# Kernel tuning notes

Hardware: AMD Instinct MI355X
Metric: run time of the kernel (lower is better)

## Reference

```python
import jax, jax.numpy as jnp
import numpy as np


def setup_inputs() -> dict:
    key = jax.random.key(0)
    k1, k2, k3 = jax.random.split(key, 3)
    B, N, M, KSUB, DSUB = 32, 1_000_000, 64, 256, 4
    querys = jax.random.normal(k1, (B, M * DSUB), dtype=jnp.float32)
    codewords = jax.random.normal(k2, (M, KSUB, DSUB), dtype=jnp.float32)
    codes = jax.random.randint(k3, (N, M), 0, KSUB, dtype=jnp.int32)
    return {"querys": querys, "codewords": codewords, "codes": codes, "k": 64}


def reference(querys, codewords, codes, k):
    """PQ asymmetric-distance (ADC) search, metric='l2'.

    querys:    (B, D) with D = M*dsub
    codewords: (M, ksub, dsub)
    codes:     (N, M) byte codes (int32 here)
    Returns (topk_distances (B,k), topk_indices (B,k)) -- smallest L2 first,
    matching faiss IndexPQ semantics.
    """
    B, D = querys.shape
    M, KSUB, DSUB = codewords.shape
    N = codes.shape[0]
    # Per-subspace squared-L2 distance table: (B, M, ksub)
    q = querys.reshape(B, M, 1, DSUB)
    table = jnp.sum((q - codewords[None]) ** 2, axis=-1)

    # ADC scan: dist[b, n] = sum_m table[b, m, codes[n, m]].
    # Loop over the M subspaces (structural dim) via lax.scan to avoid
    # materializing a (B, N, M) intermediate.
    table_m_first = jnp.transpose(table, (1, 0, 2))  # (M, B, ksub)
    codes_m_first = codes.T                          # (M, N)

    def step(acc, inp):
        t_m, c_m = inp  # (B, ksub), (N,)
        return acc + t_m[:, c_m], None  # gather -> (B, N)

    init = jnp.zeros((B, N), dtype=querys.dtype)
    dists, _ = jax.lax.scan(step, init, (table_m_first, codes_m_first))

    neg_top, idx = jax.lax.top_k(-dists, k)  # k nearest (smallest L2)
    return -neg_top, idx
```

## Files before the change

### kernel.cpp

```cpp
#include <hip/hip_runtime.h>
#include <cstdint>


#define BQ 32
#define MSUB 64
#define KSUB 256
#define DSUB 4
#define KOUT 64
#define NSAMP 16384
#define TAU_RANK 24
#define CAP 16384
#define NSORT 4096

__global__ __launch_bounds__(256) void build_table(const float* __restrict__ q,
                                                   const float* __restrict__ cw,
                                                   float* __restrict__ table) {
    int tid = blockIdx.x * 256 + threadIdx.x;
    int b = tid & 31;
    int c = (tid >> 5) & 255;
    int m = tid >> 13;
    const float* qp = q + b * (MSUB * DSUB) + m * DSUB;
    const float* cp = cw + (m * KSUB + c) * DSUB;
    float s = 0.f;
#pragma unroll
    for (int d = 0; d < DSUB; ++d) { float t = qp[d] - cp[d]; s += t * t; }
    table[tid] = s;
}

__global__ __launch_bounds__(256) void sample_dists(const float* __restrict__ table,
                                                    const int* __restrict__ codes,
                                                    float* __restrict__ samp,
                                                    int stride, int offset) {
    int j = blockIdx.x * 256 + threadIdx.x;
    int n = j * stride + offset;
    const int* crow = codes + (long)n * MSUB;
    float acc[BQ];
#pragma unroll
    for (int b = 0; b < BQ; ++b) acc[b] = 0.f;
    for (int m = 0; m < MSUB; ++m) {
        int c = crow[m];
        const float* t = table + (m * KSUB + c) * BQ;
#pragma unroll
        for (int b = 0; b < BQ; ++b) acc[b] += t[b];
    }
#pragma unroll
    for (int b = 0; b < BQ; ++b) samp[b * NSAMP + j] = acc[b];
}

__global__ __launch_bounds__(256) void find_tau(const float* __restrict__ samp,
                                                float* __restrict__ tau) {
    __shared__ uint32_t sbits[NSAMP];
    __shared__ int scount;
    int b = blockIdx.x;
    for (int i = threadIdx.x; i < NSAMP; i += 256)
        sbits[i] = __float_as_uint(samp[b * NSAMP + i]);
    __syncthreads();
    uint32_t lo = 0u, hi = 0x7F800000u;
    for (int it = 0; it < 31; ++it) {
        uint32_t mid = (lo + hi) >> 1;
        if (threadIdx.x == 0) scount = 0;
        __syncthreads();
        int c = 0;
        for (int i = threadIdx.x; i < NSAMP; i += 256) c += (sbits[i] <= mid) ? 1 : 0;
        atomicAdd(&scount, c);
        __syncthreads();
        int cnt = scount;
        __syncthreads();
        if (cnt >= TAU_RANK) hi = mid; else lo = mid;
    }
    if (threadIdx.x == 0) tau[b] = __uint_as_float(hi);
}

__global__ __launch_bounds__(256) void scan_collect(const float* __restrict__ table,
                                                    const int* __restrict__ codes,
                                                    const float* __restrict__ tau,
                                                    int* __restrict__ cnt,
                                                    int* __restrict__ cidx,
                                                    float* __restrict__ cdist,
                                                    int N) {
    int tid = blockIdx.x * 256 + threadIdx.x;
    int n = tid >> 3;
    if (n >= N) return;
    int q4 = tid & 7;
    const int* crow = codes + (long)n * MSUB;
    const float4* t4 = (const float4*)table;
    float4 acc = {0.f, 0.f, 0.f, 0.f};
#pragma unroll 8
    for (int m = 0; m < MSUB; ++m) {
        int c = crow[m];
        float4 v = t4[(m * KSUB + c) * 8 + q4];
        acc.x += v.x; acc.y += v.y; acc.z += v.z; acc.w += v.w;
    }
    float d[4] = {acc.x, acc.y, acc.z, acc.w};
    int b0 = q4 * 4;
#pragma unroll
    for (int j = 0; j < 4; ++j) {
        int b = b0 + j;
        if (d[j] <= tau[b]) {
            int pos = atomicAdd(&cnt[b], 1);
            if (pos < CAP) { cidx[b * CAP + pos] = n; cdist[b * CAP + pos] = d[j]; }
        }
    }
}

__global__ __launch_bounds__(256) void final_topk(const int* __restrict__ cnt,
                                                  const int* __restrict__ cidx,
                                                  const float* __restrict__ cdist,
                                                  float* __restrict__ out) {
    __shared__ unsigned long long keys[NSORT];
    int b = blockIdx.x;
    int m = cnt[b];
    if (m > NSORT) m = NSORT;
    for (int i = threadIdx.x; i < NSORT; i += 256) {
        unsigned long long k;
        if (i < m)
            k = ((unsigned long long)__float_as_uint(cdist[b * CAP + i]) << 32) |
                (unsigned int)cidx[b * CAP + i];
        else
            k = ~0ULL;
        keys[i] = k;
    }
    __syncthreads();
    for (int kk = 2; kk <= NSORT; kk <<= 1) {
        for (int j = kk >> 1; j > 0; j >>= 1) {
            for (int i = threadIdx.x; i < NSORT; i += 256) {
                int ixj = i ^ j;
                if (ixj > i) {
                    unsigned long long a = keys[i], c = keys[ixj];
                    bool up = ((i & kk) == 0);
                    if ((a > c) == up) { keys[i] = c; keys[ixj] = a; }
                }
            }
            __syncthreads();
        }
    }
    for (int r = threadIdx.x; r < KOUT; r += 256) {
        unsigned long long k = keys[r];
        out[b * KOUT + r] = __uint_as_float((unsigned int)(k >> 32));
        out[BQ * KOUT + b * KOUT + r] = (float)(unsigned int)(k & 0xFFFFFFFFu);
    }
}

extern "C" void kernel_launch(void* const* d_in, const int* in_sizes, int n_in,
                              void* d_out, int out_size, void* d_ws, size_t ws_size,
                              hipStream_t stream) {
    const float* querys    = (const float*)d_in[0];
    const float* codewords = (const float*)d_in[1];
    const int*   codes     = (const int*)d_in[2];
    float* out = (float*)d_out;
    int N = in_sizes[2] / MSUB;

    char* ws = (char*)d_ws;
    float* table = (float*)(ws);
    float* samp  = (float*)(ws + (2u << 20));
    float* tau   = (float*)(ws + (4u << 20));
    int*   cnt   = (int*)  (ws + (4u << 20) + 4096);
    int*   cidx  = (int*)  (ws + (4u << 20) + 8192);
    float* cdist = (float*)(ws + (6u << 20) + 8192);

    hipMemsetAsync(cnt, 0, BQ * sizeof(int), stream);

    build_table<<<(MSUB * KSUB * BQ) / 256, 256, 0, stream>>>(querys, codewords, table);

    int stride = N / NSAMP;
    int offset = 17;
    sample_dists<<<NSAMP / 256, 256, 0, stream>>>(table, codes, samp, stride, offset);

    find_tau<<<BQ, 256, 0, stream>>>(samp, tau);

    long total = (long)N * 8;
    int blocks = (int)((total + 255) / 256);
    scan_collect<<<blocks, 256, 0, stream>>>(table, codes, tau, cnt, cidx, cdist, N);

    final_topk<<<BQ, 256, 0, stream>>>(cnt, cidx, cdist, out);
}
```

Baseline: 653.8 us.

## Use 8-bit quantized LDS lookup tables with SWAR coarse scan plus exact refine

The codes are repacked into a transposed byte layout each call. The distance table is quantized to 8-bit per subspace and query, and the full scan becomes an LDS-resident SWAR filter: two 16-bit lanes are accumulated per 32-bit word, and each candidate is compared against a quantized, slack-padded threshold. Surviving candidates are rescored exactly from the float table before the final bitonic sort. This aims to replace the costly per-row global float4 gathers with cheap shared-memory byte lookups, at the cost of extra passes over the codes. It also risks exceeding the candidate cap, because quantization slack lets extra candidates through the coarse filter.

```diff
diff --git a/kernel.cpp b/kernel.cpp
--- a/kernel.cpp
+++ b/kernel.cpp
@@ -7,10 +7,26 @@
 #define KSUB 256
 #define DSUB 4
 #define KOUT 64
-#define NSAMP 16384
-#define TAU_RANK 24
-#define CAP 16384
-#define NSORT 4096
+#define NSAMP 8192
+#define TAU_RANK 12
+#define CAP 8192
+#define NSORT 8192
+#define CHUNK_N 2048
+
+__device__ __forceinline__ unsigned pack4(int4 a) {
+    return (unsigned)(a.x & 255) | ((unsigned)(a.y & 255) << 8) |
+           ((unsigned)(a.z & 255) << 16) | ((unsigned)(a.w & 255) << 24);
+}
+__global__ __launch_bounds__(256) void pack_codes_t(const int4* __restrict__ c4,
+                                                    uint4* __restrict__ PT, int N) {
+    int t = blockIdx.x * 256 + threadIdx.x;
+    if (t >= N * 4) return;
+    int n = t >> 2, w = t & 3;
+    const int4* src = c4 + ((long)n * 16 + w * 4);
+    uint4 r;
+    r.x = pack4(src[0]); r.y = pack4(src[1]); r.z = pack4(src[2]); r.w = pack4(src[3]);
+    PT[(long)(n >> 6) * 256 + w * 64 + (n & 63)] = r;
+}
 
 __global__ __launch_bounds__(256) void build_table(const float* __restrict__ q,
                                                    const float* __restrict__ cw,
@@ -27,6 +43,66 @@
     table[tid] = s;
 }
 
+__global__ __launch_bounds__(256) void minmax_kernel(const float* __restrict__ table,
+                                                     float* __restrict__ off,
+                                                     unsigned* __restrict__ maxr) {
+    int m = blockIdx.x >> 5, b = blockIdx.x & 31;
+    int c = threadIdx.x;
+    float v = table[(m * 256 + c) * 32 + b];
+    __shared__ float smin[256], smax[256];
+    smin[c] = v; smax[c] = v;
+    __syncthreads();
+    for (int s = 128; s > 0; s >>= 1) {
+        if (c < s) {
+            smin[c] = fminf(smin[c], smin[c + s]);
+            smax[c] = fmaxf(smax[c], smax[c + s]);
+        }
+        __syncthreads();
+    }
+    if (c == 0) {
+        off[m * 32 + b] = smin[0];
+        atomicMax(&maxr[b], __float_as_uint(smax[0] - smin[0]));
+    }
+}
+
+__global__ __launch_bounds__(64) void scale_kernel(const float* __restrict__ off,
+                                                   const unsigned* __restrict__ maxr,
+                                                   float* __restrict__ sVal,
+                                                   float* __restrict__ OFFv) {
+    int b = threadIdx.x;
+    if (b >= BQ) return;
+    float r = __uint_as_float(maxr[b]);
+    if (r < 1e-20f) r = 1e-20f;
+    sVal[b] = 254.5f / r;
+    float o = 0.f;
+    for (int m = 0; m < MSUB; ++m) o += off[m * 32 + b];
+    OFFv[b] = o;
+}
+
+__global__ __launch_bounds__(256) void quantize_table(const float* __restrict__ table,
+                                                      const float* __restrict__ off,
+                                                      const float* __restrict__ sVal,
+                                                      unsigned* __restrict__ qg) {
+    int m = blockIdx.x, c = threadIdx.x;
+    const float* t = table + (m * 256 + c) * 32;
+    unsigned q[32];
+#pragma unroll
+    for (int b = 0; b < 32; ++b) {
+        float x = floorf((t[b] - off[m * 32 + b]) * sVal[b]);
+        int qi = (int)x;
+        if (qi < 0) qi = 0;
+        if (qi > 255) qi = 255;
+        q[b] = (unsigned)qi;
+    }
+#pragma unroll
+    for (int o = 0; o < 4; ++o) {
+        unsigned A = q[o*8+0] | (q[o*8+1] << 8) | (q[o*8+2] << 16) | (q[o*8+3] << 24);
+        unsigned B = q[o*8+4] | (q[o*8+5] << 8) | (q[o*8+6] << 16) | (q[o*8+7] << 24);
+        qg[(2 * o + 0) * 16384 + m * 256 + c] = A;
+        qg[(2 * o + 1) * 16384 + m * 256 + c] = B;
+    }
+}
+
 __global__ __launch_bounds__(256) void sample_dists(const float* __restrict__ table,
                                                     const int* __restrict__ codes,
                                                     float* __restrict__ samp,
@@ -49,15 +125,15 @@
 
 __global__ __launch_bounds__(256) void find_tau(const float* __restrict__ samp,
                                                 float* __restrict__ tau) {
-    __shared__ uint32_t sbits[NSAMP];
+    __shared__ unsigned sbits[NSAMP];
     __shared__ int scount;
     int b = blockIdx.x;
     for (int i = threadIdx.x; i < NSAMP; i += 256)
         sbits[i] = __float_as_uint(samp[b * NSAMP + i]);
     __syncthreads();
-    uint32_t lo = 0u, hi = 0x7F800000u;
+    unsigned lo = 0u, hi = 0x7F800000u;
     for (int it = 0; it < 31; ++it) {
-        uint32_t mid = (lo + hi) >> 1;
+        unsigned mid = (lo + hi) >> 1;
         if (threadIdx.x == 0) scount = 0;
         __syncthreads();
         int c = 0;
@@ -71,36 +147,118 @@
     if (threadIdx.x == 0) tau[b] = __uint_as_float(hi);
 }
 
-__global__ __launch_bounds__(256) void scan_collect(const float* __restrict__ table,
-                                                    const int* __restrict__ codes,
-                                                    const float* __restrict__ tau,
-                                                    int* __restrict__ cnt,
-                                                    int* __restrict__ cidx,
-                                                    float* __restrict__ cdist,
-                                                    int N) {
-    int tid = blockIdx.x * 256 + threadIdx.x;
-    int n = tid >> 3;
-    if (n >= N) return;
-    int q4 = tid & 7;
-    const int* crow = codes + (long)n * MSUB;
-    const float4* t4 = (const float4*)table;
-    float4 acc = {0.f, 0.f, 0.f, 0.f};
-#pragma unroll 8
-    for (int m = 0; m < MSUB; ++m) {
-        int c = crow[m];
-        float4 v = t4[(m * KSUB + c) * 8 + q4];
-        acc.x += v.x; acc.y += v.y; acc.z += v.z; acc.w += v.w;
-    }
-    float d[4] = {acc.x, acc.y, acc.z, acc.w};
-    int b0 = q4 * 4;
-#pragma unroll
-    for (int j = 0; j < 4; ++j) {
-        int b = b0 + j;
-        if (d[j] <= tau[b]) {
-            int pos = atomicAdd(&cnt[b], 1);
-            if (pos < CAP) { cidx[b * CAP + pos] = n; cdist[b * CAP + pos] = d[j]; }
-        }
-    }
+__global__ __launch_bounds__(64) void qtau_kernel(const float* __restrict__ tau,
+                                                  const float* __restrict__ sVal,
+                                                  const float* __restrict__ OFFv,
+                                                  unsigned* __restrict__ Qt) {
+    int b = threadIdx.x;
+    if (b >= BQ) return;
+    float x = (tau[b] - OFFv[b]) * sVal[b];
+    int q = (int)floorf(x) + 8;
+    if (q < 0) q = 0;
+    if (q > 65535) q = 65535;
+    Qt[b] = (unsigned)q;
+}
+
+__global__ __launch_bounds__(512) void coarse_scan(const unsigned* __restrict__ qg,
+                                                   const uint4* __restrict__ PT,
+                                                   const unsigned* __restrict__ Qt,
+                                                   int* __restrict__ cnt,
+                                                   int* __restrict__ cidx,
+                                                   int N) {
+    __shared__ unsigned qlds[32768];
+    int o = blockIdx.y;
+    {
+        const uint4* src = (const uint4*)(qg + 2 * o * 16384);
+        uint4* dst = (uint4*)qlds;
+        for (int i = threadIdx.x; i < 8192; i += 512) dst[i] = src[i];
+    }
+    unsigned Tp0, Tp1, Tp2, Tp3, Tp4, Tp5, Tp6, Tp7;
+    {
+        const unsigned* qb = Qt + o * 8;
+        Tp0 = min(qb[0] + 1u, 32767u); Tp1 = min(qb[1] + 1u, 32767u);
+        Tp2 = min(qb[2] + 1u, 32767u); Tp3 = min(qb[3] + 1u, 32767u);
+        Tp4 = min(qb[4] + 1u, 32767u); Tp5 = min(qb[5] + 1u, 32767u);
+        Tp6 = min(qb[6] + 1u, 32767u); Tp7 = min(qb[7] + 1u, 32767u);
+    }
+    unsigned TloA = Tp0 | (Tp2 << 16), ThiA = Tp1 | (Tp3 << 16);
+    unsigned TloB = Tp4 | (Tp6 << 16), ThiB = Tp5 | (Tp7 << 16);
+    __syncthreads();
+
+    int n0 = blockIdx.x * CHUNK_N;
+    for (int i = threadIdx.x; i < CHUNK_N; i += 512) {
+        int n = n0 + i;
+        if (n >= N) break;
+        const uint4* p = PT + ((long)(n >> 6) * 256 + (n & 63));
+        uint4 w0 = p[0], w1 = p[64], w2 = p[128], w3 = p[192];
+        unsigned cw[16] = {w0.x, w0.y, w0.z, w0.w, w1.x, w1.y, w1.z, w1.w,
+                           w2.x, w2.y, w2.z, w2.w, w3.x, w3.y, w3.z, w3.w};
+        unsigned a0 = 0, a1 = 0, a2 = 0, a3 = 0;
+#pragma unroll
+        for (int w = 0; w < 16; ++w) {
+            unsigned word = cw[w];
+#pragma unroll
+            for (int k = 0; k < 4; ++k) {
+                int m = w * 4 + k;
+                unsigned c = (word >> (8 * k)) & 255u;
+                unsigned vA = qlds[m * 256 + c];
+                unsigned vB = qlds[16384 + m * 256 + c];
+                a0 += vA & 0x00FF00FFu;
+                a1 += (vA >> 8) & 0x00FF00FFu;
+                a2 += vB & 0x00FF00FFu;
+                a3 += (vB >> 8) & 0x00FF00FFu;
+            }
+        }
+        unsigned d0 = (a0 | 0x80008000u) - TloA;
+        unsigned d1 = (a1 | 0x80008000u) - ThiA;
+        unsigned d2 = (a2 | 0x80008000u) - TloB;
+        unsigned d3 = (a3 | 0x80008000u) - ThiB;
+        unsigned any = (~d0 | ~d1 | ~d2 | ~d3) & 0x80008000u;
+        if (any) {
+#pragma unroll
+            for (int j = 0; j < 8; ++j) {
+                unsigned src = (j < 4) ? ((j & 1) ? a1 : a0) : ((j & 1) ? a3 : a2);
+                unsigned v = (j & 2) ? (src >> 16) : (src & 0xFFFFu);
+                unsigned T = (j == 0) ? Tp0 : (j == 1) ? Tp1 : (j == 2) ? Tp2 :
+                             (j == 3) ? Tp3 : (j == 4) ? Tp4 : (j == 5) ? Tp5 :
+                             (j == 6) ? Tp6 : Tp7;
+                if (v < T) {
+                    int b = o * 8 + j;
+                    int pos = atomicAdd(&cnt[b], 1);
+                    if (pos < CAP) cidx[b * CAP + pos] = n;
+                }
+            }
+        }
+    }
+}
+
+__global__ __launch_bounds__(256) void refine(const float* __restrict__ table,
+                                              const uint4* __restrict__ PT,
+                                              const int* __restrict__ cnt,
+                                              const int* __restrict__ cidx,
+                                              float* __restrict__ cdist) {
+    int b = blockIdx.y;
+    int pos = blockIdx.x * 256 + threadIdx.x;
+    int mc = cnt[b]; if (mc > CAP) mc = CAP;
+    if (pos >= mc) return;
+    int n = cidx[b * CAP + pos];
+    const uint4* p = PT + ((long)(n >> 6) * 256 + (n & 63));
+    uint4 w0 = p[0], w1 = p[64], w2 = p[128], w3 = p[192];
+    unsigned cw[16] = {w0.x, w0.y, w0.z, w0.w, w1.x, w1.y, w1.z, w1.w,
+                       w2.x, w2.y, w2.z, w2.w, w3.x, w3.y, w3.z, w3.w};
+    float s = 0.f;
+    const float* tb = table + b;
+#pragma unroll
+    for (int w = 0; w < 16; ++w) {
+        unsigned word = cw[w];
+#pragma unroll
+        for (int k = 0; k < 4; ++k) {
+            unsigned c = (word >> (8 * k)) & 255u;
+            int m = w * 4 + k;
+            s += tb[(m * 256 + c) * 32];
+        }
+    }
+    cdist[b * CAP + pos] = s;
 }
 
 __global__ __launch_bounds__(256) void final_topk(const int* __restrict__ cnt,
@@ -115,7 +273,7 @@
         unsigned long long k;
         if (i < m)
             k = ((unsigned long long)__float_as_uint(cdist[b * CAP + i]) << 32) |
-                (unsigned int)cidx[b * CAP + i];
+                (unsigned)cidx[b * CAP + i];
         else
             k = ~0ULL;
         keys[i] = k;
@@ -136,8 +294,8 @@
     }
     for (int r = threadIdx.x; r < KOUT; r += 256) {
         unsigned long long k = keys[r];
-        out[b * KOUT + r] = __uint_as_float((unsigned int)(k >> 32));
-        out[BQ * KOUT + b * KOUT + r] = (float)(unsigned int)(k & 0xFFFFFFFFu);
+        out[b * KOUT + r] = __uint_as_float((unsigned)(k >> 32));
+        out[BQ * KOUT + b * KOUT + r] = (float)(unsigned)(k & 0xFFFFFFFFu);
     }
 }
 
@@ -151,26 +309,42 @@
     int N = in_sizes[2] / MSUB;
 
     char* ws = (char*)d_ws;
-    float* table = (float*)(ws);
-    float* samp  = (float*)(ws + (2u << 20));
-    float* tau   = (float*)(ws + (4u << 20));
-    int*   cnt   = (int*)  (ws + (4u << 20) + 4096);
-    int*   cidx  = (int*)  (ws + (4u << 20) + 8192);
-    float* cdist = (float*)(ws + (6u << 20) + 8192);
-
-    hipMemsetAsync(cnt, 0, BQ * sizeof(int), stream);
+    float*    table = (float*)(ws);
+    float*    samp  = (float*)(ws + (2u << 20));
+    char*     small = ws + (3u << 20);
+    float*    tau   = (float*)(small + 0);
+    float*    sVal  = (float*)(small + 128);
+    float*    OFFv  = (float*)(small + 256);
+    unsigned* Qt    = (unsigned*)(small + 384);
+    int*      cnt   = (int*)(small + 512);
+    unsigned* maxr  = (unsigned*)(small + 640);
+    float*    off   = (float*)(small + 1024);
+    unsigned* qg    = (unsigned*)(small + 16384);
+    int*      cidx  = (int*)(ws + (4u << 20));
+    float*    cdist = (float*)(ws + (5u << 20));
+    uint4*    PT    = (uint4*)(ws + (6u << 20));
+
+    hipMemsetAsync(small + 512, 0, 256, stream);
+
+    pack_codes_t<<<(N * 4) / 256 + 1, 256, 0, stream>>>((const int4*)codes, PT, N);
 
     build_table<<<(MSUB * KSUB * BQ) / 256, 256, 0, stream>>>(querys, codewords, table);
+
+    minmax_kernel<<<MSUB * BQ, 256, 0, stream>>>(table, off, maxr);
+    scale_kernel<<<1, 64, 0, stream>>>(off, maxr, sVal, OFFv);
+    quantize_table<<<MSUB, 256, 0, stream>>>(table, off, sVal, qg);
 
     int stride = N / NSAMP;
     int offset = 17;
     sample_dists<<<NSAMP / 256, 256, 0, stream>>>(table, codes, samp, stride, offset);
-
     find_tau<<<BQ, 256, 0, stream>>>(samp, tau);
-
-    long total = (long)N * 8;
-    int blocks = (int)((total + 255) / 256);
-    scan_collect<<<blocks, 256, 0, stream>>>(table, codes, tau, cnt, cidx, cdist, N);
+    qtau_kernel<<<1, 64, 0, stream>>>(tau, sVal, OFFv, Qt);
+
+    dim3 cgrid((N + CHUNK_N - 1) / CHUNK_N, 4);
+    coarse_scan<<<cgrid, 512, 0, stream>>>(qg, PT, Qt, cnt, cidx, N);
+
+    dim3 rgrid(CAP / 256, BQ);
+    refine<<<rgrid, 256, 0, stream>>>(table, PT, cnt, cidx, cdist);
 
     final_topk<<<BQ, 256, 0, stream>>>(cnt, cidx, cdist, out);
 }
```

New measurement: 1.519 ms. +132.3%, slower.
